# Kernel optimization log

Measured on AMD Instinct MI355X. Metric: run time of the kernel, lower is better.

## Reference

```python
import jax, jax.numpy as jnp
import numpy as np

N, E, G = 50000, 400000, 2048
H, C = 4, 64            # heads, hidden per head
IN, ED, TASKS = 29, 6, 12
HC = H * C


def setup_inputs() -> dict:
    key = jax.random.key(0)
    ks = jax.random.split(key, 20)
    s = 0.1
    f32 = jnp.float32
    inp = {
        'x': jax.random.normal(ks[0], (N, IN), f32),
        'edge_index': jax.random.randint(ks[1], (2, E), 0, N),
        'edge_attr': jax.random.normal(ks[2], (E, ED), f32),
        'batch': jnp.sort(jax.random.randint(ks[3], (N,), 0, G)),
        # layer 1 (in=29 -> H*C=256)
        'W1': jax.random.normal(ks[4], (IN, HC), f32) * s,
        'as1': jax.random.normal(ks[5], (1, H, C), f32) * s,
        'ad1': jax.random.normal(ks[6], (1, H, C), f32) * s,
        'We1': jax.random.normal(ks[7], (ED, HC), f32) * s,
        'ae1': jax.random.normal(ks[8], (1, H, C), f32) * s,
        'b1': jnp.zeros((HC,), f32),
        # layer 2 (in=256 -> 256)
        'W2': jax.random.normal(ks[9], (HC, HC), f32) * s,
        'as2': jax.random.normal(ks[10], (1, H, C), f32) * s,
        'ad2': jax.random.normal(ks[11], (1, H, C), f32) * s,
        'We2': jax.random.normal(ks[12], (ED, HC), f32) * s,
        'ae2': jax.random.normal(ks[13], (1, H, C), f32) * s,
        'b2': jnp.zeros((HC,), f32),
        # readout linear (256 -> 12)
        'Wl': jax.random.normal(ks[14], (HC, TASKS), f32) * s,
        'bl': jnp.zeros((TASKS,), f32),
    }
    return inp


def _gat_conv(x, src, dst, eattr, W, a_src, a_dst, We, a_e, b):
    """PyG GATConv, concat=True, leaky_relu slope 0.2, self-loops already appended."""
    h = (x @ W).reshape(N, H, C)                      # [N,H,C]
    al_s = jnp.sum(h * a_src, axis=-1)                # [N,H]
    al_d = jnp.sum(h * a_dst, axis=-1)                # [N,H]
    he = (eattr @ We).reshape(-1, H, C)               # [Etot,H,C]
    al_e = jnp.sum(he * a_e, axis=-1)                 # [Etot,H]
    alpha = al_s[src] + al_d[dst] + al_e              # [Etot,H]
    alpha = jax.nn.leaky_relu(alpha, negative_slope=0.2)
    # segment softmax over incoming edges of each dst node
    amax = jax.ops.segment_max(alpha, dst, num_segments=N)
    ex = jnp.exp(alpha - amax[dst])
    denom = jax.ops.segment_sum(ex, dst, num_segments=N)
    alpha = ex / (denom[dst] + 1e-16)
    msg = h[src] * alpha[:, :, None]                  # [Etot,H,C]
    out = jax.ops.segment_sum(msg, dst, num_segments=N)
    return out.reshape(N, HC) + b


def reference(x, edge_index, edge_attr, batch,
              W1, as1, ad1, We1, ae1, b1,
              W2, as2, ad2, We2, ae2, b2, Wl, bl):
    # add self-loops with edge_attr fill = mean over existing edges (PyG default)
    loop = jnp.arange(N)
    src = jnp.concatenate([edge_index[0], loop])
    dst = jnp.concatenate([edge_index[1], loop])
    mean_e = jnp.mean(edge_attr, axis=0, keepdims=True)
    eattr = jnp.concatenate([edge_attr, jnp.broadcast_to(mean_e, (N, ED))], axis=0)

    h = _gat_conv(x, src, dst, eattr, W1, as1, ad1, We1, ae1, b1)
    h = jax.nn.relu(h)
    h = _gat_conv(h, src, dst, eattr, W2, as2, ad2, We2, ae2, b2)
    h = jax.nn.relu(h)

    # global mean pool over graphs
    sums = jax.ops.segment_sum(h, batch, num_segments=G)      # [G,HC]
    cnt = jax.ops.segment_sum(jnp.ones((N,), h.dtype), batch, num_segments=G)
    pooled = sums / jnp.maximum(cnt, 1.0)[:, None]
    return pooled @ Wl + bl
```

## Files before the change

### kernel.cpp

```cpp
#include <hip/hip_runtime.h>
#include <math.h>

static constexpr int NN = 50000;
static constexpr int EE = 400000;
static constexpr int GG = 2048;
static constexpr int TASKS = 12;

typedef __attribute__((ext_vector_type(8))) short short8;
typedef __attribute__((ext_vector_type(4))) float floatx4;

__device__ __forceinline__ unsigned short f2bf(float f) {
  unsigned u = __float_as_uint(f);
  u = u + 0x7fffu + ((u >> 16) & 1u);
  return (unsigned short)(u >> 16);
}
__device__ __forceinline__ float bflo(unsigned u) { return __uint_as_float(u << 16); }
__device__ __forceinline__ float bfhi(unsigned u) { return __uint_as_float(u & 0xffff0000u); }

static constexpr int NBDEG = (EE + 255) / 256;
static constexpr int NBMEAN = 256;
static constexpr int NBX = (NN * 4 + 255) / 256;
static constexpr int NW1 = 32;
static constexpr int NW2 = 256;
__global__ void k_pre(const int* __restrict__ dst, const float* __restrict__ ea,
                      const float* __restrict__ x, const float* __restrict__ W1,
                      const float* __restrict__ W2, int* __restrict__ deg,
                      float* __restrict__ msum, unsigned short* __restrict__ xb,
                      unsigned short* __restrict__ w1t, unsigned short* __restrict__ w2t) {
  const int b = blockIdx.x;
  const int t = threadIdx.x;
  if (b < NBDEG) {
    int e = b * 256 + t;
    if (e < EE) atomicAdd(&deg[dst[e]], 1);
  } else if (b < NBDEG + NBMEAN) {
    float s[6] = {0, 0, 0, 0, 0, 0};
    for (int e = (b - NBDEG) * 256 + t; e < EE; e += NBMEAN * 256) {
#pragma unroll
      for (int d = 0; d < 6; d++) s[d] += ea[(size_t)e * 6 + d];
    }
    __shared__ float ls[6];
    if (t < 6) ls[t] = 0.f;
    __syncthreads();
#pragma unroll
    for (int d = 0; d < 6; d++) atomicAdd(&ls[d], s[d]);
    __syncthreads();
    if (t < 6) atomicAdd(&msum[t], ls[t]);
  } else if (b < NBDEG + NBMEAN + NBX) {
    int i = (b - NBDEG - NBMEAN) * 256 + t;
    if (i < NN * 4) {
      int n = i >> 2, seg = i & 3;
      unsigned short v[8];
#pragma unroll
      for (int j = 0; j < 8; j++) {
        int k = seg * 8 + j;
        v[j] = (k < 29) ? f2bf(x[(size_t)n * 29 + k]) : (unsigned short)0;
      }
      *(short8*)(xb + (size_t)n * 32 + seg * 8) = *(short8*)v;
    }
  } else if (b < NBDEG + NBMEAN + NBX + NW1) {
    int i = (b - NBDEG - NBMEAN - NBX) * 256 + t;
    int n = i >> 5, k = i & 31;
    w1t[i] = (k < 29) ? f2bf(W1[(size_t)k * 256 + n]) : (unsigned short)0;
  } else {
    int i = (b - NBDEG - NBMEAN - NBX - NW1) * 256 + t;
    int n = i >> 8, k = i & 255;
    w2t[i] = f2bf(W2[(size_t)k * 256 + n]);
  }
}

__global__ void k_scan1(const int* __restrict__ deg, int* __restrict__ rowptr, int* __restrict__ bsums) {
  __shared__ int sh[256];
  int i = blockIdx.x * 256 + threadIdx.x;
  int v = (i < NN) ? deg[i] : 0;
  sh[threadIdx.x] = v;
  __syncthreads();
  for (int off = 1; off < 256; off <<= 1) {
    int t = (threadIdx.x >= off) ? sh[threadIdx.x - off] : 0;
    __syncthreads();
    sh[threadIdx.x] += t;
    __syncthreads();
  }
  if (i < NN) rowptr[i] = sh[threadIdx.x] - v;
  if (threadIdx.x == 255) bsums[blockIdx.x] = sh[255];
}

__global__ void k_scan23(int* __restrict__ rowptr, const int* __restrict__ bsums, int nb) {
  __shared__ int sh[256];
  const int t = threadIdx.x;
  sh[t] = (t < nb) ? bsums[t] : 0;
  __syncthreads();
  for (int off = 1; off < 256; off <<= 1) {
    int tv = (t >= off) ? sh[t - off] : 0;
    __syncthreads();
    sh[t] += tv;
    __syncthreads();
  }
  const int add = (blockIdx.x == 0) ? 0 : sh[blockIdx.x - 1];
  int i = blockIdx.x * 256 + t;
  if (i < NN) rowptr[i] += add;
  if (i == 0) rowptr[NN] = EE;
}

__global__ void k_scatparams(const int* __restrict__ ei, const int* __restrict__ rowptr,
                             int* __restrict__ cursor, int* __restrict__ csrc,
                             int* __restrict__ eslot, const float* __restrict__ We1,
                             const float* __restrict__ ae1, const float* __restrict__ We2,
                             const float* __restrict__ ae2, const float* __restrict__ msum,
                             float* __restrict__ p1, float* __restrict__ p2) {
  const int b = blockIdx.x;
  const int t = threadIdx.x;
  if (b < NBDEG) {
    int e = b * 256 + t;
    if (e >= EE) return;
    int s = ei[e];
    int d = ei[EE + e];
    int p = atomicAdd(&cursor[d], 1);
    int slot = rowptr[d] + p;
    csrc[slot] = s;
    eslot[e] = slot;
  } else {
    const int layer = b - NBDEG;
    const float* We = layer ? We2 : We1;
    const float* ae = layer ? ae2 : ae1;
    float* params = layer ? p2 : p1;
    __shared__ float vsh[24];
    if (t < 24) {
      int d = t >> 2, h = t & 3;
      float s = 0.f;
      for (int c = 0; c < 64; c++) s += We[d * 256 + h * 64 + c] * ae[h * 64 + c];
      vsh[t] = s;
      params[t] = s;
    }
    __syncthreads();
    if (t < 4) {
      float s = 0.f;
      const float invE = 1.0f / (float)EE;
#pragma unroll
      for (int d = 0; d < 6; d++) s += (msum[d] * invE) * vsh[d * 4 + t];
      params[24 + t] = s;
    }
  }
}

template <int KP>
__global__ __launch_bounds__(256, 3) void k_gemm_mfma(
    const unsigned short* __restrict__ A, const unsigned short* __restrict__ Bt,
    const float* __restrict__ a_s, const float* __restrict__ a_d,
    unsigned short* __restrict__ Y, float* __restrict__ als, float* __restrict__ ald,
    int M) {
  const int tid = threadIdx.x;
  const int lane = tid & 63;
  const int w = tid >> 6;
  const int l15 = lane & 15;
  const int quad = lane >> 4;
  const int row0 = blockIdx.x * 64;

  floatx4 acc[4][4];
#pragma unroll
  for (int i = 0; i < 4; i++)
#pragma unroll
    for (int j = 0; j < 4; j++) acc[i][j] = {0.f, 0.f, 0.f, 0.f};

  const unsigned short* pa[4];
  const unsigned short* pb[4];
#pragma unroll
  for (int i = 0; i < 4; i++) {
    int r = row0 + i * 16 + l15;
    if (r >= M) r = M - 1;
    pa[i] = A + (size_t)r * KP + quad * 8;
  }
#pragma unroll
  for (int j = 0; j < 4; j++) pb[j] = Bt + (size_t)(w * 64 + j * 16 + l15) * KP + quad * 8;

  constexpr int NPH = KP / 32;
  short8 af[2][4], bfr[2][4];
#pragma unroll
  for (int i = 0; i < 4; i++) af[0][i] = *(const short8*)pa[i];
#pragma unroll
  for (int j = 0; j < 4; j++) bfr[0][j] = *(const short8*)pb[j];
#pragma unroll
  for (int ph = 0; ph < NPH; ph++) {
    const int cur = ph & 1, nxt = cur ^ 1;
    if (ph + 1 < NPH) {
#pragma unroll
      for (int i = 0; i < 4; i++) {
        pa[i] += 32;
        af[nxt][i] = *(const short8*)pa[i];
      }
#pragma unroll
      for (int j = 0; j < 4; j++) {
        pb[j] += 32;
        bfr[nxt][j] = *(const short8*)pb[j];
      }
    }
#pragma unroll
    for (int i = 0; i < 4; i++)
#pragma unroll
      for (int j = 0; j < 4; j++)
        acc[i][j] = __builtin_amdgcn_mfma_f32_16x16x32_bf16(af[cur][i], bfr[cur][j], acc[i][j], 0, 0, 0);
  }
  float asc[4], adc[4];
#pragma unroll
  for (int j = 0; j < 4; j++) {
    asc[j] = a_s[w * 64 + j * 16 + l15];
    adc[j] = a_d[w * 64 + j * 16 + l15];
  }
#pragma unroll
  for (int i = 0; i < 4; i++) {
#pragma unroll
    for (int r = 0; r < 4; r++) {
      const int row = row0 + i * 16 + quad * 4 + r;
      unsigned ub[4];
      float hv[4];
#pragma unroll
      for (int j = 0; j < 4; j++) {
        ub[j] = f2bf(acc[i][j][r]);
        hv[j] = __uint_as_float(ub[j] << 16);
      }
      if (row < M) {
#pragma unroll
        for (int j = 0; j < 4; j++) Y[(size_t)row * 256 + w * 64 + j * 16 + l15] = (unsigned short)ub[j];
      }
      float ps = hv[0] * asc[0] + hv[1] * asc[1] + hv[2] * asc[2] + hv[3] * asc[3];
      float pd = hv[0] * adc[0] + hv[1] * adc[1] + hv[2] * adc[2] + hv[3] * adc[3];
#pragma unroll
      for (int off = 1; off < 16; off <<= 1) {
        ps += __shfl_xor(ps, off, 64);
        pd += __shfl_xor(pd, off, 64);
      }
      if (l15 == 0 && row < M) {
        als[row * 4 + w] = ps;
        ald[row * 4 + w] = pd;
      }
    }
  }
}

__device__ __forceinline__ float leaky02(float x) { return x > 0.f ? x : 0.2f * x; }

__global__ void k_edge(const int* __restrict__ ei, const float* __restrict__ ea,
                       const float* __restrict__ als, const float* __restrict__ ald,
                       const int* __restrict__ eslot, const float* __restrict__ params,
                       float* __restrict__ exa) {
  int e = blockIdx.x * blockDim.x + threadIdx.x;
  if (e >= EE) return;
  int src = ei[e], dst = ei[EE + e];
  float4 s4 = *(const float4*)(als + (size_t)src * 4);
  float4 d4 = *(const float4*)(ald + (size_t)dst * 4);
  float ed[6];
#pragma unroll
  for (int d = 0; d < 6; d++) ed[d] = ea[(size_t)e * 6 + d];
  float sl[4] = {s4.x + d4.x, s4.y + d4.y, s4.z + d4.z, s4.w + d4.w};
  float out[4];
#pragma unroll
  for (int h = 0; h < 4; h++) {
    float x = sl[h];
#pragma unroll
    for (int d = 0; d < 6; d++) x += ed[d] * params[d * 4 + h];
    out[h] = __expf(leaky02(x));
  }
  *(float4*)(exa + (size_t)eslot[e] * 4) = make_float4(out[0], out[1], out[2], out[3]);
}

__global__ __launch_bounds__(256) void k_agg(
    const unsigned short* __restrict__ hinb, const float* __restrict__ als,
    const float* __restrict__ ald, const int* __restrict__ rowptr, const int* __restrict__ csrc,
    const float* __restrict__ exa, const float* __restrict__ params, const float* __restrict__ bias,
    unsigned short* __restrict__ houtb) {
  const int lane = threadIdx.x & 63;
  const int n = blockIdx.x * 4 + (threadIdx.x >> 6);
  if (n >= NN) return;
  const int half = lane >> 5;
  const int sl = lane & 31;
  const int head = sl >> 3;

  float acc[8];
  float ssum;
  {
    float slg = leaky02(als[n * 4 + head] + ald[n * 4 + head] + params[24 + head]);
    float exs = __expf(slg);
    float wgt = (half == 0) ? exs : 0.f;
    ssum = wgt;
    uint4 uv = *(const uint4*)(hinb + (size_t)n * 256 + sl * 8);
    acc[0] = bflo(uv.x) * wgt;
    acc[1] = bfhi(uv.x) * wgt;
    acc[2] = bflo(uv.y) * wgt;
    acc[3] = bfhi(uv.y) * wgt;
    acc[4] = bflo(uv.z) * wgt;
    acc[5] = bfhi(uv.z) * wgt;
    acc[6] = bflo(uv.w) * wgt;
    acc[7] = bfhi(uv.w) * wgt;
  }
  const int end = rowptr[n + 1];
  int s = rowptr[n] + half;
  int sn = 0;
  float ex = 0.f;
  if (s < end) {
    sn = csrc[s];
    ex = exa[(size_t)s * 4 + head];
  }
  while (s < end) {
    const int sc = sn;
    const float exc = ex;
    const int s2 = s + 2;
    if (s2 < end) {
      sn = csrc[s2];
      ex = exa[(size_t)s2 * 4 + head];
    }
    uint4 uv = *(const uint4*)(hinb + (size_t)sc * 256 + sl * 8);
    acc[0] += bflo(uv.x) * exc;
    acc[1] += bfhi(uv.x) * exc;
    acc[2] += bflo(uv.y) * exc;
    acc[3] += bfhi(uv.y) * exc;
    acc[4] += bflo(uv.z) * exc;
    acc[5] += bfhi(uv.z) * exc;
    acc[6] += bflo(uv.w) * exc;
    acc[7] += bfhi(uv.w) * exc;
    ssum += exc;
    s = s2;
  }
#pragma unroll
  for (int j = 0; j < 8; j++) acc[j] += __shfl_xor(acc[j], 32, 64);
  ssum += __shfl_xor(ssum, 32, 64);
  if (half == 0) {
    const float inv = 1.f / (ssum + 1e-16f);
    float4 b0 = *(const float4*)(bias + sl * 8);
    float4 b1 = *(const float4*)(bias + sl * 8 + 4);
    const float bb[8] = {b0.x, b0.y, b0.z, b0.w, b1.x, b1.y, b1.z, b1.w};
    uint p[4];
#pragma unroll
    for (int j = 0; j < 4; j++) {
      float e0 = fmaxf(acc[2 * j] * inv + bb[2 * j], 0.f);
      float e1 = fmaxf(acc[2 * j + 1] * inv + bb[2 * j + 1], 0.f);
      p[j] = (uint)f2bf(e0) | ((uint)f2bf(e1) << 16);
    }
    *(uint4*)(houtb + (size_t)n * 256 + sl * 8) = make_uint4(p[0], p[1], p[2], p[3]);
  }
}

__global__ __launch_bounds__(256) void k_pool(const unsigned short* __restrict__ hb,
                                              const int* __restrict__ batch,
                                              const float* __restrict__ Wl,
                                              const float* __restrict__ bl,
                                              float* __restrict__ out) {
  int g = blockIdx.x;
  int t = threadIdx.x;
  int lo = 0, hi = NN;
  while (lo < hi) {
    int mid = (lo + hi) >> 1;
    if (batch[mid] < g) lo = mid + 1; else hi = mid;
  }
  int start = lo;
  hi = NN;
  while (lo < hi) {
    int mid = (lo + hi) >> 1;
    if (batch[mid] < g + 1) lo = mid + 1; else hi = mid;
  }
  int end = lo;
  __shared__ float sp[256];
  if (t < 128) {
    float s0 = 0.f, s1 = 0.f;
    for (int n2 = start; n2 < end; n2++) {
      uint u = ((const uint*)(hb + (size_t)n2 * 256))[t];
      s0 += bflo(u);
      s1 += bfhi(u);
    }
    float invc = 1.f / fmaxf((float)(end - start), 1.f);
    sp[2 * t] = s0 * invc;
    sp[2 * t + 1] = s1 * invc;
  }
  __syncthreads();
  if (t < TASKS) {
    float o = bl[t];
    for (int c = 0; c < 256; c++) o += sp[c] * Wl[c * 12 + t];
    out[(size_t)g * 12 + t] = o;
  }
}

extern "C" void kernel_launch(void* const* d_in, const int* in_sizes, int n_in,
                              void* d_out, int out_size, void* d_ws, size_t ws_size,
                              hipStream_t stream) {
  const float* x = (const float*)d_in[0];
  const int* ei = (const int*)d_in[1];
  const float* ea = (const float*)d_in[2];
  const int* batch = (const int*)d_in[3];
  const float* W1 = (const float*)d_in[4];
  const float* as1 = (const float*)d_in[5];
  const float* ad1 = (const float*)d_in[6];
  const float* We1 = (const float*)d_in[7];
  const float* ae1 = (const float*)d_in[8];
  const float* b1 = (const float*)d_in[9];
  const float* W2 = (const float*)d_in[10];
  const float* as2 = (const float*)d_in[11];
  const float* ad2 = (const float*)d_in[12];
  const float* We2 = (const float*)d_in[13];
  const float* ae2 = (const float*)d_in[14];
  const float* b2 = (const float*)d_in[15];
  const float* Wl = (const float*)d_in[16];
  const float* bl = (const float*)d_in[17];
  float* out = (float*)d_out;

  char* ws = (char*)d_ws;
  size_t off = 0;
  auto take = [&](size_t bytes) -> char* {
    char* p = ws + off;
    off = (off + bytes + 255) & ~(size_t)255;
    return p;
  };
  float* msum = (float*)take(8 * 4);
  int* deg = (int*)take((size_t)NN * 4);
  int* cursor = (int*)take((size_t)NN * 4);
  size_t zero_end = off;
  int* rowptr = (int*)take((size_t)(NN + 1) * 4);
  int* bsums = (int*)take(256 * 4);
  int* csrc = (int*)take((size_t)EE * 4);
  int* eslot = (int*)take((size_t)EE * 4);
  float* exa = (float*)take((size_t)EE * 4 * 4);
  float* p1 = (float*)take(32 * 4);
  float* p2 = (float*)take(32 * 4);
  float* als = (float*)take((size_t)NN * 4 * 4);
  float* ald = (float*)take((size_t)NN * 4 * 4);
  unsigned short* hb = (unsigned short*)take((size_t)NN * 256 * 2);
  unsigned short* ab = (unsigned short*)take((size_t)NN * 256 * 2);
  unsigned short* xb = (unsigned short*)take((size_t)NN * 32 * 2);
  unsigned short* w1t = (unsigned short*)take((size_t)256 * 32 * 2);
  unsigned short* w2t = (unsigned short*)take((size_t)256 * 256 * 2);
  (void)ws_size;

  hipMemsetAsync(ws, 0, zero_end, stream);

  const int nbN = (NN + 255) / 256;
  const int nbE = (EE + 255) / 256;

  k_pre<<<NBDEG + NBMEAN + NBX + NW1 + NW2, 256, 0, stream>>>(ei + EE, ea, x, W1, W2,
                                                              deg, msum, xb, w1t, w2t);
  k_scan1<<<nbN, 256, 0, stream>>>(deg, rowptr, bsums);
  k_scan23<<<nbN, 256, 0, stream>>>(rowptr, bsums, nbN);
  k_scatparams<<<NBDEG + 2, 256, 0, stream>>>(ei, rowptr, cursor, csrc, eslot,
                                              We1, ae1, We2, ae2, msum, p1, p2);

  const int gb = (NN + 63) / 64;

  k_gemm_mfma<32><<<gb, 256, 0, stream>>>(xb, w1t, as1, ad1, hb, als, ald, NN);
  k_edge<<<nbE, 256, 0, stream>>>(ei, ea, als, ald, eslot, p1, exa);
  k_agg<<<NN / 4, 256, 0, stream>>>(hb, als, ald, rowptr, csrc, exa, p1, b1, ab);

  k_gemm_mfma<256><<<gb, 256, 0, stream>>>(ab, w2t, as2, ad2, hb, als, ald, NN);
  k_edge<<<nbE, 256, 0, stream>>>(ei, ea, als, ald, eslot, p2, exa);
  k_agg<<<NN / 4, 256, 0, stream>>>(hb, als, ald, rowptr, csrc, exa, p2, b2, ab);

  k_pool<<<GG, 256, 0, stream>>>(ab, batch, Wl, bl, out);
}
```

Before: 330.3 us.

## Fuse CSR scatter with layer-1 GEMM and pre-tile weights for coalesced fragment loads

Merges the edge-scatter/param kernel with the layer-1 MFMA GEMM into one launch, so the independent scatter and GEMM blocks run concurrently and one launch is removed. Transposed bf16 weights are now stored in a 16x8 fragment-tiled layout, so each wave's B-fragment loads are contiguous 256-byte chunks instead of strided rows. Launch bounds occupancy hint drops from 3 to 2 blocks per CU, which may reduce occupancy.

```diff
diff --git a/kernel.cpp b/kernel.cpp
--- a/kernel.cpp
+++ b/kernel.cpp
@@ -59,12 +59,13 @@
     }
   } else if (b < NBDEG + NBMEAN + NBX + NW1) {
     int i = (b - NBDEG - NBMEAN - NBX) * 256 + t;
-    int n = i >> 5, k = i & 31;
-    w1t[i] = (k < 29) ? f2bf(W1[(size_t)k * 256 + n]) : (unsigned short)0;
+    int row = i >> 5, k = i & 31;
+    unsigned short v = (k < 29) ? f2bf(W1[(size_t)k * 256 + row]) : (unsigned short)0;
+    w1t[((row >> 4) * 4 + (k >> 3)) * 128 + (row & 15) * 8 + (k & 7)] = v;
   } else {
     int i = (b - NBDEG - NBMEAN - NBX - NW1) * 256 + t;
-    int n = i >> 8, k = i & 255;
-    w2t[i] = f2bf(W2[(size_t)k * 256 + n]);
+    int row = i >> 8, k = i & 255;
+    w2t[((row >> 4) * 32 + (k >> 3)) * 128 + (row & 15) * 8 + (k & 7)] = f2bf(W2[(size_t)k * 256 + row]);
   }
 }
 
@@ -101,12 +102,110 @@
   if (i == 0) rowptr[NN] = EE;
 }
 
-__global__ void k_scatparams(const int* __restrict__ ei, const int* __restrict__ rowptr,
-                             int* __restrict__ cursor, int* __restrict__ csrc,
-                             int* __restrict__ eslot, const float* __restrict__ We1,
-                             const float* __restrict__ ae1, const float* __restrict__ We2,
-                             const float* __restrict__ ae2, const float* __restrict__ msum,
-                             float* __restrict__ p1, float* __restrict__ p2) {
+template <int KP>
+__device__ __forceinline__ void gemm_body(
+    int bx, const unsigned short* __restrict__ A, const unsigned short* __restrict__ Bt,
+    const float* __restrict__ a_s, const float* __restrict__ a_d,
+    unsigned short* __restrict__ Y, float* __restrict__ als, float* __restrict__ ald, int M) {
+  const int tid = threadIdx.x;
+  const int lane = tid & 63;
+  const int w = tid >> 6;
+  const int l15 = lane & 15;
+  const int quad = lane >> 4;
+  const int row0 = bx * 64;
+
+  floatx4 acc[4][4];
+#pragma unroll
+  for (int i = 0; i < 4; i++)
+#pragma unroll
+    for (int j = 0; j < 4; j++) acc[i][j] = {0.f, 0.f, 0.f, 0.f};
+
+  const unsigned short* pa[4];
+  const unsigned short* pb[4];
+#pragma unroll
+  for (int i = 0; i < 4; i++) {
+    int r = row0 + i * 16 + l15;
+    if (r >= M) r = M - 1;
+    pa[i] = A + (size_t)r * KP + quad * 8;
+  }
+#pragma unroll
+  for (int j = 0; j < 4; j++)
+    pb[j] = Bt + (size_t)((w * 4 + j) * (KP / 8) + quad) * 128 + l15 * 8;
+
+  constexpr int NPH = KP / 32;
+  short8 af[2][4], bfr[2][4];
+#pragma unroll
+  for (int i = 0; i < 4; i++) af[0][i] = *(const short8*)pa[i];
+#pragma unroll
+  for (int j = 0; j < 4; j++) bfr[0][j] = *(const short8*)pb[j];
+#pragma unroll
+  for (int ph = 0; ph < NPH; ph++) {
+    const int cur = ph & 1, nxt = cur ^ 1;
+    if (ph + 1 < NPH) {
+#pragma unroll
+      for (int i = 0; i < 4; i++) {
+        pa[i] += 32;
+        af[nxt][i] = *(const short8*)pa[i];
+      }
+#pragma unroll
+      for (int j = 0; j < 4; j++) {
+        pb[j] += 512;
+        bfr[nxt][j] = *(const short8*)pb[j];
+      }
+    }
+#pragma unroll
+    for (int i = 0; i < 4; i++)
+#pragma unroll
+      for (int j = 0; j < 4; j++)
+        acc[i][j] = __builtin_amdgcn_mfma_f32_16x16x32_bf16(af[cur][i], bfr[cur][j], acc[i][j], 0, 0, 0);
+  }
+  float asc[4], adc[4];
+#pragma unroll
+  for (int j = 0; j < 4; j++) {
+    asc[j] = a_s[w * 64 + j * 16 + l15];
+    adc[j] = a_d[w * 64 + j * 16 + l15];
+  }
+#pragma unroll
+  for (int i = 0; i < 4; i++) {
+#pragma unroll
+    for (int r = 0; r < 4; r++) {
+      const int row = row0 + i * 16 + quad * 4 + r;
+      unsigned ub[4];
+      float hv[4];
+#pragma unroll
+      for (int j = 0; j < 4; j++) {
+        ub[j] = f2bf(acc[i][j][r]);
+        hv[j] = __uint_as_float(ub[j] << 16);
+      }
+      if (row < M) {
+#pragma unroll
+        for (int j = 0; j < 4; j++) Y[(size_t)row * 256 + w * 64 + j * 16 + l15] = (unsigned short)ub[j];
+      }
+      float ps = hv[0] * asc[0] + hv[1] * asc[1] + hv[2] * asc[2] + hv[3] * asc[3];
+      float pd = hv[0] * adc[0] + hv[1] * adc[1] + hv[2] * adc[2] + hv[3] * adc[3];
+#pragma unroll
+      for (int off = 1; off < 16; off <<= 1) {
+        ps += __shfl_xor(ps, off, 64);
+        pd += __shfl_xor(pd, off, 64);
+      }
+      if (l15 == 0 && row < M) {
+        als[row * 4 + w] = ps;
+        ald[row * 4 + w] = pd;
+      }
+    }
+  }
+}
+
+static constexpr int GB = (NN + 63) / 64;
+
+__global__ __launch_bounds__(256, 2) void k_scatgemm1(
+    const int* __restrict__ ei, const int* __restrict__ rowptr, int* __restrict__ cursor,
+    int* __restrict__ csrc, int* __restrict__ eslot, const float* __restrict__ We1,
+    const float* __restrict__ ae1, const float* __restrict__ We2, const float* __restrict__ ae2,
+    const float* __restrict__ msum, float* __restrict__ p1, float* __restrict__ p2,
+    const unsigned short* __restrict__ xb, const unsigned short* __restrict__ w1t,
+    const float* __restrict__ as1, const float* __restrict__ ad1,
+    unsigned short* __restrict__ hb, float* __restrict__ als, float* __restrict__ ald) {
   const int b = blockIdx.x;
   const int t = threadIdx.x;
   if (b < NBDEG) {
@@ -118,7 +217,7 @@
     int slot = rowptr[d] + p;
     csrc[slot] = s;
     eslot[e] = slot;
-  } else {
+  } else if (b < NBDEG + 2) {
     const int layer = b - NBDEG;
     const float* We = layer ? We2 : We1;
     const float* ae = layer ? ae2 : ae1;
@@ -139,101 +238,16 @@
       for (int d = 0; d < 6; d++) s += (msum[d] * invE) * vsh[d * 4 + t];
       params[24 + t] = s;
     }
-  }
-}
-
-template <int KP>
-__global__ __launch_bounds__(256, 3) void k_gemm_mfma(
+  } else {
+    gemm_body<32>(b - NBDEG - 2, xb, w1t, as1, ad1, hb, als, ald, NN);
+  }
+}
+
+__global__ __launch_bounds__(256, 2) void k_gemm2(
     const unsigned short* __restrict__ A, const unsigned short* __restrict__ Bt,
     const float* __restrict__ a_s, const float* __restrict__ a_d,
-    unsigned short* __restrict__ Y, float* __restrict__ als, float* __restrict__ ald,
-    int M) {
-  const int tid = threadIdx.x;
-  const int lane = tid & 63;
-  const int w = tid >> 6;
-  const int l15 = lane & 15;
-  const int quad = lane >> 4;
-  const int row0 = blockIdx.x * 64;
-
-  floatx4 acc[4][4];
-#pragma unroll
-  for (int i = 0; i < 4; i++)
-#pragma unroll
-    for (int j = 0; j < 4; j++) acc[i][j] = {0.f, 0.f, 0.f, 0.f};
-
-  const unsigned short* pa[4];
-  const unsigned short* pb[4];
-#pragma unroll
-  for (int i = 0; i < 4; i++) {
-    int r = row0 + i * 16 + l15;
-    if (r >= M) r = M - 1;
-    pa[i] = A + (size_t)r * KP + quad * 8;
-  }
-#pragma unroll
-  for (int j = 0; j < 4; j++) pb[j] = Bt + (size_t)(w * 64 + j * 16 + l15) * KP + quad * 8;
-
-  constexpr int NPH = KP / 32;
-  short8 af[2][4], bfr[2][4];
-#pragma unroll
-  for (int i = 0; i < 4; i++) af[0][i] = *(const short8*)pa[i];
-#pragma unroll
-  for (int j = 0; j < 4; j++) bfr[0][j] = *(const short8*)pb[j];
-#pragma unroll
-  for (int ph = 0; ph < NPH; ph++) {
-    const int cur = ph & 1, nxt = cur ^ 1;
-    if (ph + 1 < NPH) {
-#pragma unroll
-      for (int i = 0; i < 4; i++) {
-        pa[i] += 32;
-        af[nxt][i] = *(const short8*)pa[i];
-      }
-#pragma unroll
-      for (int j = 0; j < 4; j++) {
-        pb[j] += 32;
-        bfr[nxt][j] = *(const short8*)pb[j];
-      }
-    }
-#pragma unroll
-    for (int i = 0; i < 4; i++)
-#pragma unroll
-      for (int j = 0; j < 4; j++)
-        acc[i][j] = __builtin_amdgcn_mfma_f32_16x16x32_bf16(af[cur][i], bfr[cur][j], acc[i][j], 0, 0, 0);
-  }
-  float asc[4], adc[4];
-#pragma unroll
-  for (int j = 0; j < 4; j++) {
-    asc[j] = a_s[w * 64 + j * 16 + l15];
-    adc[j] = a_d[w * 64 + j * 16 + l15];
-  }
-#pragma unroll
-  for (int i = 0; i < 4; i++) {
-#pragma unroll
-    for (int r = 0; r < 4; r++) {
-      const int row = row0 + i * 16 + quad * 4 + r;
-      unsigned ub[4];
-      float hv[4];
-#pragma unroll
-      for (int j = 0; j < 4; j++) {
-        ub[j] = f2bf(acc[i][j][r]);
-        hv[j] = __uint_as_float(ub[j] << 16);
-      }
-      if (row < M) {
-#pragma unroll
-        for (int j = 0; j < 4; j++) Y[(size_t)row * 256 + w * 64 + j * 16 + l15] = (unsigned short)ub[j];
-      }
-      float ps = hv[0] * asc[0] + hv[1] * asc[1] + hv[2] * asc[2] + hv[3] * asc[3];
-      float pd = hv[0] * adc[0] + hv[1] * adc[1] + hv[2] * adc[2] + hv[3] * adc[3];
-#pragma unroll
-      for (int off = 1; off < 16; off <<= 1) {
-        ps += __shfl_xor(ps, off, 64);
-        pd += __shfl_xor(pd, off, 64);
-      }
-      if (l15 == 0 && row < M) {
-        als[row * 4 + w] = ps;
-        ald[row * 4 + w] = pd;
-      }
-    }
-  }
+    unsigned short* __restrict__ Y, float* __restrict__ als, float* __restrict__ ald) {
+  gemm_body<256>(blockIdx.x, A, Bt, a_s, a_d, Y, als, ald, NN);
 }
 
 __device__ __forceinline__ float leaky02(float x) { return x > 0.f ? x : 0.2f * x; }
@@ -436,16 +450,15 @@
                                                               deg, msum, xb, w1t, w2t);
   k_scan1<<<nbN, 256, 0, stream>>>(deg, rowptr, bsums);
   k_scan23<<<nbN, 256, 0, stream>>>(rowptr, bsums, nbN);
-  k_scatparams<<<NBDEG + 2, 256, 0, stream>>>(ei, rowptr, cursor, csrc, eslot,
-                                              We1, ae1, We2, ae2, msum, p1, p2);
-
-  const int gb = (NN + 63) / 64;
-
-  k_gemm_mfma<32><<<gb, 256, 0, stream>>>(xb, w1t, as1, ad1, hb, als, ald, NN);
+
+  k_scatgemm1<<<NBDEG + 2 + GB, 256, 0, stream>>>(ei, rowptr, cursor, csrc, eslot,
+                                                  We1, ae1, We2, ae2, msum, p1, p2,
+                                                  xb, w1t, as1, ad1, hb, als, ald);
+
   k_edge<<<nbE, 256, 0, stream>>>(ei, ea, als, ald, eslot, p1, exa);
   k_agg<<<NN / 4, 256, 0, stream>>>(hb, als, ald, rowptr, csrc, exa, p1, b1, ab);
 
-  k_gemm_mfma<256><<<gb, 256, 0, stream>>>(ab, w2t, as2, ad2, hb, als, ald, NN);
+  k_gemm2<<<GB, 256, 0, stream>>>(ab, w2t, as2, ad2, hb, als, ald);
   k_edge<<<nbE, 256, 0, stream>>>(ei, ea, als, ald, eslot, p2, exa);
   k_agg<<<NN / 4, 256, 0, stream>>>(hb, als, ald, rowptr, csrc, exa, p2, b2, ab);
 
```

New measurement: 315.2 us. 1.05x faster.
